# Performance work log

Measured on AMD Instinct MI355X. Metric: run time of the kernel, lower is better.

## Reference

```python
import jax, jax.numpy as jnp
import numpy as np

N_NODES = 50000
N_EDGES = 800000
N_GRAPHS = 2000
D_NODE = 64
D_EDGE = 16
D_MID = 128
N_LAYERS = 3
BN_EPS = 1e-5
LRELU_SLOPE = 0.01


def _bn(h, g, b):
    # training-mode BatchNorm1d: biased batch stats over node dim
    m = jnp.mean(h, axis=0)
    v = jnp.mean((h - m) ** 2, axis=0)
    return (h - m) * jax.lax.rsqrt(v + BN_EPS) * g + b


def _lrelu(h):
    return jnp.where(h >= 0, h, LRELU_SLOPE * h)


def setup_inputs() -> dict:
    key = jax.random.key(0)
    ks = jax.random.split(key, 16)
    s = 0.05
    inp = {
        'x': jax.random.normal(ks[0], (N_NODES, D_NODE), jnp.float32),
        'edge_attr': jax.random.normal(ks[1], (N_EDGES, D_EDGE), jnp.float32),
        'lin_edge_W': jax.random.normal(ks[2], (N_LAYERS, D_EDGE, D_NODE), jnp.float32) * s,
        'lin_edge_b': jax.random.normal(ks[3], (N_LAYERS, D_NODE), jnp.float32) * s,
        'W1': jax.random.normal(ks[4], (N_LAYERS, D_NODE, D_NODE), jnp.float32) * s,
        'b1': jax.random.normal(ks[5], (N_LAYERS, D_NODE), jnp.float32) * s,
        'bn1_g': jnp.ones((N_LAYERS, D_NODE), jnp.float32),
        'bn1_b': jnp.zeros((N_LAYERS, D_NODE), jnp.float32),
        'W2': jax.random.normal(ks[6], (N_LAYERS, D_NODE, D_NODE), jnp.float32) * s,
        'b2': jax.random.normal(ks[7], (N_LAYERS, D_NODE), jnp.float32) * s,
        'eps': jnp.zeros((N_LAYERS,), jnp.float32),
        'obn_g': jnp.ones((N_LAYERS, D_NODE), jnp.float32),
        'obn_b': jnp.zeros((N_LAYERS, D_NODE), jnp.float32),
        'cW1': jax.random.normal(ks[8], (2 * D_NODE, D_MID), jnp.float32) * s,
        'cb1': jax.random.normal(ks[9], (D_MID,), jnp.float32) * s,
        'cbn1_g': jnp.ones((D_MID,), jnp.float32),
        'cbn1_b': jnp.zeros((D_MID,), jnp.float32),
        'cW2': jax.random.normal(ks[10], (D_MID, D_MID), jnp.float32) * s,
        'cb2': jax.random.normal(ks[11], (D_MID,), jnp.float32) * s,
        'cbn2_g': jnp.ones((D_MID,), jnp.float32),
        'cbn2_b': jnp.zeros((D_MID,), jnp.float32),
        'cW3': jax.random.normal(ks[12], (D_MID, 1), jnp.float32) * s,
        'cb3': jax.random.normal(ks[13], (1,), jnp.float32) * s,
        'edge_index': jax.random.randint(ks[14], (2, N_EDGES), 0, N_NODES, jnp.int64 if jax.config.jax_enable_x64 else jnp.int32),
        'batch': jnp.sort(jax.random.randint(ks[15], (N_NODES,), 0, N_GRAPHS, jnp.int64 if jax.config.jax_enable_x64 else jnp.int32)),
    }
    return inp


def reference(x, edge_attr, lin_edge_W, lin_edge_b, W1, b1, bn1_g, bn1_b, W2, b2,
              eps, obn_g, obn_b, cW1, cb1, cbn1_g, cbn1_b, cW2, cb2, cbn2_g,
              cbn2_b, cW3, cb3, edge_index, batch):
    src = edge_index[0]  # source nodes j
    dst = edge_index[1]  # target nodes i
    for l in range(N_LAYERS):
        e = edge_attr @ lin_edge_W[l] + lin_edge_b[l]          # [E, D]
        msg = jax.nn.relu(x[src] + e)                          # [E, D]
        aggr = jax.ops.segment_sum(msg, dst, num_segments=N_NODES)
        h = (1.0 + eps[l]) * x + aggr
        h = _lrelu(_bn(h @ W1[l] + b1[l], bn1_g[l], bn1_b[l])) @ W2[l] + b2[l]
        if l != N_LAYERS - 1:
            h = _bn(h, obn_g[l], obn_b[l])
        x = _lrelu(h)
    pool = jax.ops.segment_sum(x, batch, num_segments=N_GRAPHS)  # [G, D]
    h = jnp.concatenate([x, pool[batch]], axis=1)                # [N, 2D]
    h = _lrelu(_bn(h @ cW1 + cb1, cbn1_g, cbn1_b))               # Dropout = identity (eval)
    h = _lrelu(_bn(h @ cW2 + cb2, cbn2_g, cbn2_b))
    out = h @ cW3 + cb3                                          # [N, 1]
    return out.reshape(-1)
```

## Files before the change

### kernel.cpp

```cpp
#include <hip/hip_runtime.h>

#define NN 50000
#define NE 800000
#define NG 2000
#define BN_EPS 1e-5f
#define NB_SCAN 196
#define NCHUNK 50000

typedef __attribute__((ext_vector_type(8))) short bf16x8;
typedef __attribute__((ext_vector_type(4))) float f32x4;

__device__ __forceinline__ float lrelu(float v) { return v > 0.f ? v : 0.01f * v; }

__device__ __forceinline__ unsigned short f2bf(float x) {
    union { float f; unsigned u; } v; v.f = x;
    unsigned r = v.u + 0x7FFF + ((v.u >> 16) & 1);
    return (unsigned short)(r >> 16);
}
__device__ __forceinline__ float bf2f(unsigned short h) {
    union { unsigned u; float f; } v; v.u = ((unsigned)h) << 16;
    return v.f;
}
__device__ __forceinline__ bf16x8 u4_to_bf(uint4 u) {
    union { uint4 q; bf16x8 b; } c; c.q = u; return c.b;
}

__global__ __launch_bounds__(256) void k_prep(int* __restrict__ p, int n)
{
    int tid = blockIdx.x * 256 + threadIdx.x;
    for (int i = tid; i < n; i += gridDim.x * 256) p[i] = 0;
}

__global__ __launch_bounds__(256) void k_wcvt(
    const float* __restrict__ W1, const float* __restrict__ W2,
    const float* __restrict__ cW1, const float* __restrict__ cW2,
    unsigned short* __restrict__ w1h, unsigned short* __restrict__ w1l,
    unsigned short* __restrict__ w2h, unsigned short* __restrict__ w2l,
    unsigned short* __restrict__ cw1h, unsigned short* __restrict__ cw1l,
    unsigned short* __restrict__ cw2h, unsigned short* __restrict__ cw2l)
{
    int b = blockIdx.x, t = threadIdx.x;
    if (b < 6) {
        const float* s = (b < 3) ? (W1 + b * 4096) : (W2 + (b - 3) * 4096);
        unsigned short* dh = (b < 3) ? (w1h + b * 4096) : (w2h + (b - 3) * 4096);
        unsigned short* dl = (b < 3) ? (w1l + b * 4096) : (w2l + (b - 3) * 4096);
        for (int i = t; i < 4096; i += 256) {
            int k = i >> 6, n = i & 63;
            float v = s[i];
            unsigned short h = f2bf(v);
            dh[n * 64 + k] = h;
            dl[n * 64 + k] = f2bf(v - bf2f(h));
        }
    } else {
        const float* s = (b == 6) ? cW1 : cW2;
        unsigned short* dh = (b == 6) ? cw1h : cw2h;
        unsigned short* dl = (b == 6) ? cw1l : cw2l;
        for (int i = t; i < 16384; i += 256) {
            int k = i >> 7, n = i & 127;
            float v = s[i];
            unsigned short h = f2bf(v);
            dh[n * 128 + k] = h;
            dl[n * 128 + k] = f2bf(v - bf2f(h));
        }
    }
}

__global__ __launch_bounds__(256) void k_hist(const int* __restrict__ dst, int* __restrict__ cnt)
{
    int tid = blockIdx.x * 256 + threadIdx.x;
    for (int e = tid; e < NE; e += gridDim.x * 256) atomicAdd(&cnt[dst[e]], 1);
}

__global__ __launch_bounds__(256) void k_scanA(const int* __restrict__ cnt,
    int* __restrict__ off, int* __restrict__ bsum)
{
    __shared__ int s[256];
    int t = threadIdx.x;
    int i = blockIdx.x * 256 + t;
    int v = (i < NN) ? cnt[i] : 0;
    s[t] = v; __syncthreads();
    #pragma unroll
    for (int d = 1; d < 256; d <<= 1) {
        int u = (t >= d) ? s[t - d] : 0;
        __syncthreads();
        s[t] += u;
        __syncthreads();
    }
    if (i < NN) off[i + 1] = s[t];
    if (t == 255) bsum[blockIdx.x] = s[255];
}

__global__ __launch_bounds__(256) void k_scanB(const int* __restrict__ bsum, int* __restrict__ boff)
{
    __shared__ int s[256];
    int t = threadIdx.x;
    int v = (t < NB_SCAN) ? bsum[t] : 0;
    s[t] = v; __syncthreads();
    #pragma unroll
    for (int d = 1; d < 256; d <<= 1) {
        int u = (t >= d) ? s[t - d] : 0;
        __syncthreads();
        s[t] += u;
        __syncthreads();
    }
    boff[t] = s[t] - v;
}

__global__ __launch_bounds__(256) void k_scanC(const int* __restrict__ cnt,
    int* __restrict__ off, const int* __restrict__ boff, int* __restrict__ cur)
{
    int i = blockIdx.x * 256 + threadIdx.x;
    if (i < NN) {
        int incl = off[i + 1] + boff[blockIdx.x];
        off[i + 1] = incl;
        cur[i] = incl - cnt[i];
    }
    if (i == 0) off[0] = 0;
}

__global__ __launch_bounds__(256) void k_scatter2(
    const int* __restrict__ src, const int* __restrict__ dst,
    int* __restrict__ cur, const float* __restrict__ ea,
    unsigned short* __restrict__ eaz)
{
    int tid = blockIdx.x * 256 + threadIdx.x;
    for (int e = tid; e < NE; e += gridDim.x * 256) {
        int s = src[e], d = dst[e];
        int p = atomicAdd(&cur[d], 1);
        const float4* ap = (const float4*)(ea + (size_t)e * 16);
        float4 a0 = ap[0], a1 = ap[1], a2 = ap[2], a3 = ap[3];
        float v[16] = {a0.x, a0.y, a0.z, a0.w, a1.x, a1.y, a1.z, a1.w,
                       a2.x, a2.y, a2.z, a2.w, a3.x, a3.y, a3.z, a3.w};
        unsigned hi[8], lo[6];
        #pragma unroll
        for (int j = 0; j < 8; ++j) {
            unsigned short h0 = f2bf(v[2 * j]), h1 = f2bf(v[2 * j + 1]);
            hi[j] = (unsigned)h0 | ((unsigned)h1 << 16);
            if (j < 6)
                lo[j] = (unsigned)f2bf(v[2 * j] - bf2f(f2bf(v[2 * j])))
                      | ((unsigned)f2bf(v[2 * j + 1] - bf2f(f2bf(v[2 * j + 1]))) << 16);
        }
        uint4* rec = (uint4*)(eaz + (size_t)p * 32);
        uint4 r0 = {hi[0], hi[1], hi[2], hi[3]};
        uint4 r1 = {hi[4], hi[5], hi[6], hi[7]};
        uint4 r2 = {lo[0], lo[1], lo[2], lo[3]};
        uint4 r3 = {lo[4], lo[5], (unsigned)s, (unsigned)d};
        rec[0] = r0; rec[1] = r1; rec[2] = r2; rec[3] = r3;
    }
}

__global__ __launch_bounds__(256) void k_init(const float* __restrict__ x,
    const float* __restrict__ eps, int layer, float* __restrict__ aggr)
{
    int tid = blockIdx.x * 256 + threadIdx.x;
    float s = 1.f + eps[layer];
    const float4* xv = (const float4*)x;
    float4* av = (float4*)aggr;
    for (int i = tid; i < NN * 16; i += gridDim.x * 256) {
        float4 v = xv[i];
        v.x *= s; v.y *= s; v.z *= s; v.w *= s;
        av[i] = v;
    }
}

__global__ __launch_bounds__(256) void k_aggr_m(
    const float* __restrict__ x, const unsigned short* __restrict__ eaz,
    const float* __restrict__ We, const float* __restrict__ be,
    float* __restrict__ aggr)
{
    __shared__ unsigned short wth[1024], wtl[1024];
    __shared__ float els[4 * 16 * 65];
    int t = threadIdx.x;
    for (int i = t; i < 1024; i += 256) {
        int col = i >> 4, k = i & 15;
        float v = We[k * 64 + col];
        unsigned short h = f2bf(v);
        wth[col * 16 + k] = h;
        wtl[col * 16 + k] = f2bf(v - bf2f(h));
    }
    __syncthreads();

    int lane = t & 63, w = t >> 6;
    float* myels = els + w * (16 * 65);
    int ar = lane & 15;
    int kg = (lane >> 4) & 1;
    bool klive = lane < 32;

    bf16x8 bh[4], bl[4];
    float bias4[4];
    #pragma unroll
    for (int nc = 0; nc < 4; ++nc) {
        int col = nc * 16 + ar;
        uint4 hv = {0, 0, 0, 0}, lv = {0, 0, 0, 0};
        if (klive) {
            hv = *(const uint4*)(wth + col * 16 + kg * 8);
            lv = *(const uint4*)(wtl + col * 16 + kg * 8);
        }
        bh[nc] = u4_to_bf(hv);
        bl[nc] = u4_to_bf(lv);
        bias4[nc] = be[col];
    }

    int cbase0 = (blockIdx.x * 4 + w) * 8;
    for (int ci = 0; ci < 8; ++ci) {
        int chunk = cbase0 + ci;
        if (chunk >= NCHUNK) break;
        int e0 = chunk * 16;
        const unsigned short* rec = eaz + (size_t)(e0 + ar) * 32;

        int2 sdv = *(const int2*)(rec + 28);
        int sl = sdv.x, dl = sdv.y;

        uint4 hv = {0, 0, 0, 0}, lv = {0, 0, 0, 0};
        if (klive) {
            hv = *(const uint4*)(rec + kg * 8);
            lv = *(const uint4*)(rec + 16 + kg * 8);
            if (kg) { lv.z = 0; lv.w = 0; }
        }
        bf16x8 ah = u4_to_bf(hv), al = u4_to_bf(lv);

        float xv[16];
        #pragma unroll
        for (int e = 0; e < 16; ++e) {
            int s_e = __builtin_amdgcn_readlane(sl, e);
            xv[e] = x[(size_t)s_e * 64 + lane];
        }

        #pragma unroll
        for (int nc = 0; nc < 4; ++nc) {
            f32x4 acc;
            acc[0] = bias4[nc]; acc[1] = bias4[nc]; acc[2] = bias4[nc]; acc[3] = bias4[nc];
            acc = __builtin_amdgcn_mfma_f32_16x16x32_bf16(ah, bh[nc], acc, 0, 0, 0);
            acc = __builtin_amdgcn_mfma_f32_16x16x32_bf16(al, bh[nc], acc, 0, 0, 0);
            acc = __builtin_amdgcn_mfma_f32_16x16x32_bf16(ah, bl[nc], acc, 0, 0, 0);
            int rbase = (lane >> 4) * 4;
            #pragma unroll
            for (int r = 0; r < 4; ++r)
                myels[(rbase + r) * 65 + nc * 16 + ar] = acc[r];
        }

        int d = __builtin_amdgcn_readlane(dl, 0);
        float acc = 0.f;
        #pragma unroll
        for (int e = 0; e < 16; ++e) {
            float m = xv[e] + myels[e * 65 + lane];
            m = fmaxf(m, 0.f);
            acc += m;
            int dn = (e < 15) ? __builtin_amdgcn_readlane(dl, e + 1) : -1;
            if (dn != d) {
                atomicAdd(&aggr[(size_t)d * 64 + lane], acc);
                acc = 0.f;
                d = dn;
            }
        }
    }
}

template<int PRE, int POST>
__global__ __launch_bounds__(256) void k_mm64_f(
    const float* __restrict__ in,
    const unsigned short* __restrict__ Wh, const unsigned short* __restrict__ Wl,
    const float* __restrict__ bias, const float* __restrict__ statsIn,
    const float* __restrict__ gIn, const float* __restrict__ bIn,
    float* __restrict__ out, float* __restrict__ statsOut,
    const int* __restrict__ batch, float* __restrict__ pool)
{
    __shared__ unsigned short Ash[64 * 64], Asl[64 * 64];
    __shared__ unsigned short Bsh[64 * 64], Bsl[64 * 64];
    __shared__ float sc[64], sh[64];
    __shared__ float red[4 * 128];
    int t = threadIdx.x;
    int base = blockIdx.x * 64;
    if (PRE && t < 64) {
        float m = statsIn[t] * (1.f / NN);
        float v = statsIn[64 + t] * (1.f / NN) - m * m;
        float s = gIn[t] * rsqrtf(v + BN_EPS);
        sc[t] = s; sh[t] = bIn[t] - m * s;
    }
    for (int i = t; i < 512; i += 256) {
        int n = i >> 3, cb = i & 7;
        ((uint4*)Bsh)[n * 8 + (cb ^ (n & 7))] = ((const uint4*)Wh)[i];
        ((uint4*)Bsl)[n * 8 + (cb ^ (n & 7))] = ((const uint4*)Wl)[i];
    }
    __syncthreads();
    for (int i = t; i < 512; i += 256) {
        int row = i >> 3, cb = i & 7;
        int node = base + row;
        float v[8] = {0.f, 0.f, 0.f, 0.f, 0.f, 0.f, 0.f, 0.f};
        if (node < NN) {
            float4 u0 = *(const float4*)(in + (size_t)node * 64 + cb * 8);
            float4 u1 = *(const float4*)(in + (size_t)node * 64 + cb * 8 + 4);
            v[0] = u0.x; v[1] = u0.y; v[2] = u0.z; v[3] = u0.w;
            v[4] = u1.x; v[5] = u1.y; v[6] = u1.z; v[7] = u1.w;
            if (PRE) {
                #pragma unroll
                for (int j = 0; j < 8; ++j) {
                    int c = cb * 8 + j;
                    v[j] = lrelu(fmaf(v[j], sc[c], sh[c]));
                }
            }
        }
        unsigned hw[4], lw[4];
        #pragma unroll
        for (int j = 0; j < 4; ++j) {
            unsigned short h0 = f2bf(v[2 * j]), h1 = f2bf(v[2 * j + 1]);
            unsigned short l0 = f2bf(v[2 * j] - bf2f(h0)), l1 = f2bf(v[2 * j + 1] - bf2f(h1));
            hw[j] = (unsigned)h0 | ((unsigned)h1 << 16);
            lw[j] = (unsigned)l0 | ((unsigned)l1 << 16);
        }
        uint4 rh = { hw[0], hw[1], hw[2], hw[3] };
        uint4 rl = { lw[0], lw[1], lw[2], lw[3] };
        int idx = row * 8 + (cb ^ (row & 7));
        ((uint4*)Ash)[idx] = rh;
        ((uint4*)Asl)[idx] = rl;
    }
    __syncthreads();

    int w = t >> 6, l = t & 63;
    int ar = l & 15, kg = l >> 4;
    bf16x8 afh[2], afl[2];
    #pragma unroll
    for (int kt = 0; kt < 2; ++kt) {
        int row = w * 16 + ar, cb = kt * 4 + kg;
        int idx = row * 8 + (cb ^ (row & 7));
        afh[kt] = ((const bf16x8*)Ash)[idx];
        afl[kt] = ((const bf16x8*)Asl)[idx];
    }
    f32x4 acc[4];
    #pragma unroll
    for (int nt = 0; nt < 4; ++nt) { acc[nt][0] = 0.f; acc[nt][1] = 0.f; acc[nt][2] = 0.f; acc[nt][3] = 0.f; }
    #pragma unroll
    for (int nt = 0; nt < 4; ++nt) {
        #pragma unroll
        for (int kt = 0; kt < 2; ++kt) {
            int n = nt * 16 + ar, cb = kt * 4 + kg;
            int idx = n * 8 + (cb ^ (n & 7));
            bf16x8 bfh = ((const bf16x8*)Bsh)[idx];
            bf16x8 bfl = ((const bf16x8*)Bsl)[idx];
            acc[nt] = __builtin_amdgcn_mfma_f32_16x16x32_bf16(afh[kt], bfh, acc[nt], 0, 0, 0);
            acc[nt] = __builtin_amdgcn_mfma_f32_16x16x32_bf16(afl[kt], bfh, acc[nt], 0, 0, 0);
            acc[nt] = __builtin_amdgcn_mfma_f32_16x16x32_bf16(afh[kt], bfl, acc[nt], 0, 0, 0);
        }
    }
    int rb = base + w * 16 + kg * 4;
    int bidx[4];
    if (POST == 1) {
        #pragma unroll
        for (int r = 0; r < 4; ++r)
            bidx[r] = (rb + r < NN) ? batch[rb + r] : 0;
    }
    #pragma unroll
    for (int nt = 0; nt < 4; ++nt) {
        int col = nt * 16 + ar;
        float bv = bias[col];
        float s = 0.f, q = 0.f;
        #pragma unroll
        for (int r = 0; r < 4; ++r) {
            int node = rb + r;
            float d = acc[nt][r] + bv;
            if (POST == 1) d = lrelu(d);
            if (node < NN) {
                out[(size_t)node * 64 + col] = d;
                if (POST == 1)
                    atomicAdd(&pool[(size_t)bidx[r] * 64 + col], d);
            }
            if (POST == 0) {
                d = (node < NN) ? d : 0.f;
                s += d; q += d * d;
            }
        }
        if (POST == 0) {
            s += __shfl_xor(s, 16); s += __shfl_xor(s, 32);
            q += __shfl_xor(q, 16); q += __shfl_xor(q, 32);
            if (kg == 0) { red[w * 128 + col] = s; red[w * 128 + 64 + col] = q; }
        }
    }
    if (POST == 0) {
        __syncthreads();
        if (t < 128) {
            int c = t & 63, which = t >> 6;
            float v = red[0 * 128 + which * 64 + c] + red[1 * 128 + which * 64 + c]
                    + red[2 * 128 + which * 64 + c] + red[3 * 128 + which * 64 + c];
            atomicAdd(&statsOut[which * 64 + c], v);
        }
    }
}

template<int MODE>
__global__ __launch_bounds__(256) void k_cmm_f(
    const float* __restrict__ inA, const float* __restrict__ pool,
    const int* __restrict__ batch, const float* __restrict__ statsIn,
    const float* __restrict__ gIn, const float* __restrict__ bIn,
    const unsigned short* __restrict__ Wh, const unsigned short* __restrict__ Wl,
    const float* __restrict__ bias,
    float* __restrict__ out, float* __restrict__ statsOut)
{
    __shared__ unsigned short Ash[64 * 128], Asl[64 * 128];
    __shared__ unsigned short Bsh[64 * 128], Bsl[64 * 128];
    __shared__ float sc[128], sh[128];
    __shared__ float red[4 * 128];
    int t = threadIdx.x;
    int base = (blockIdx.x >> 1) * 64;
    int ncol0 = (blockIdx.x & 1) * 64;
    if (MODE == 1 && t < 128) {
        float m = statsIn[t] * (1.f / NN);
        float v = statsIn[128 + t] * (1.f / NN) - m * m;
        float s = gIn[t] * rsqrtf(v + BN_EPS);
        sc[t] = s; sh[t] = bIn[t] - m * s;
    }
    for (int i = t; i < 1024; i += 256) {
        int n = i >> 4, cb = i & 15;
        int idx = n * 16 + (cb ^ (n & 7));
        ((uint4*)Bsh)[idx] = ((const uint4*)Wh)[(ncol0 + n) * 16 + cb];
        ((uint4*)Bsl)[idx] = ((const uint4*)Wl)[(ncol0 + n) * 16 + cb];
    }
    __syncthreads();
    for (int i = t; i < 1024; i += 256) {
        int row = i >> 4, cb = i & 15;
        int node = base + row;
        float v[8] = {0.f, 0.f, 0.f, 0.f, 0.f, 0.f, 0.f, 0.f};
        if (node < NN) {
            const float* sp;
            if (MODE == 0) {
                sp = (cb < 8) ? (inA + (size_t)node * 64 + cb * 8)
                              : (pool + (size_t)batch[node] * 64 + (cb - 8) * 8);
            } else {
                sp = inA + (size_t)node * 128 + cb * 8;
            }
            float4 u0 = *(const float4*)sp;
            float4 u1 = *(const float4*)(sp + 4);
            v[0] = u0.x; v[1] = u0.y; v[2] = u0.z; v[3] = u0.w;
            v[4] = u1.x; v[5] = u1.y; v[6] = u1.z; v[7] = u1.w;
            if (MODE == 1) {
                #pragma unroll
                for (int j = 0; j < 8; ++j) {
                    int c = cb * 8 + j;
                    v[j] = lrelu(fmaf(v[j], sc[c], sh[c]));
                }
            }
        }
        unsigned hw[4], lw[4];
        #pragma unroll
        for (int j = 0; j < 4; ++j) {
            unsigned short h0 = f2bf(v[2 * j]), h1 = f2bf(v[2 * j + 1]);
            unsigned short l0 = f2bf(v[2 * j] - bf2f(h0)), l1 = f2bf(v[2 * j + 1] - bf2f(h1));
            hw[j] = (unsigned)h0 | ((unsigned)h1 << 16);
            lw[j] = (unsigned)l0 | ((unsigned)l1 << 16);
        }
        uint4 rh = { hw[0], hw[1], hw[2], hw[3] };
        uint4 rl = { lw[0], lw[1], lw[2], lw[3] };
        int idx = row * 16 + (cb ^ (row & 7));
        ((uint4*)Ash)[idx] = rh;
        ((uint4*)Asl)[idx] = rl;
    }
    __syncthreads();

    int w = t >> 6, l = t & 63;
    int ar = l & 15, kg = l >> 4;
    bf16x8 afh[4], afl[4];
    #pragma unroll
    for (int kt = 0; kt < 4; ++kt) {
        int row = w * 16 + ar, cb = kt * 4 + kg;
        int idx = row * 16 + (cb ^ (row & 7));
        afh[kt] = ((const bf16x8*)Ash)[idx];
        afl[kt] = ((const bf16x8*)Asl)[idx];
    }
    f32x4 acc[4];
    #pragma unroll
    for (int nt = 0; nt < 4; ++nt) { acc[nt][0] = 0.f; acc[nt][1] = 0.f; acc[nt][2] = 0.f; acc[nt][3] = 0.f; }
    #pragma unroll
    for (int nt = 0; nt < 4; ++nt) {
        #pragma unroll
        for (int kt = 0; kt < 4; ++kt) {
            int n = nt * 16 + ar, cb = kt * 4 + kg;
            int idx = n * 16 + (cb ^ (n & 7));
            bf16x8 bfh = ((const bf16x8*)Bsh)[idx];
            bf16x8 bfl = ((const bf16x8*)Bsl)[idx];
            acc[nt] = __builtin_amdgcn_mfma_f32_16x16x32_bf16(afh[kt], bfh, acc[nt], 0, 0, 0);
            acc[nt] = __builtin_amdgcn_mfma_f32_16x16x32_bf16(afl[kt], bfh, acc[nt], 0, 0, 0);
            acc[nt] = __builtin_amdgcn_mfma_f32_16x16x32_bf16(afh[kt], bfl, acc[nt], 0, 0, 0);
        }
    }
    int rb = base + w * 16 + kg * 4;
    #pragma unroll
    for (int nt = 0; nt < 4; ++nt) {
        int colg = ncol0 + nt * 16 + ar;
        float bv = bias[colg];
        float s = 0.f, q = 0.f;
        #pragma unroll
        for (int r = 0; r < 4; ++r) {
            int node = rb + r;
            float d = acc[nt][r] + bv;
            if (node < NN) out[(size_t)node * 128 + colg] = d;
            d = (node < NN) ? d : 0.f;
            s += d; q += d * d;
        }
        s += __shfl_xor(s, 16); s += __shfl_xor(s, 32);
        q += __shfl_xor(q, 16); q += __shfl_xor(q, 32);
        int col = nt * 16 + ar;
        if (kg == 0) { red[w * 128 + col] = s; red[w * 128 + 64 + col] = q; }
    }
    __syncthreads();
    if (t < 128) {
        int c = t & 63, which = t >> 6;
        float v = red[0 * 128 + which * 64 + c] + red[1 * 128 + which * 64 + c]
                + red[2 * 128 + which * 64 + c] + red[3 * 128 + which * 64 + c];
        atomicAdd(&statsOut[which * 128 + ncol0 + c], v);
    }
}

__global__ __launch_bounds__(256) void k_bn2(
    const float* __restrict__ in, const float* __restrict__ stats,
    const float* __restrict__ g, const float* __restrict__ b,
    const float* __restrict__ eps, int nextLayer,
    float* __restrict__ xout, float* __restrict__ aggrOut)
{
    int tid = blockIdx.x * 256 + threadIdx.x;
    float e1 = 1.f + eps[nextLayer];
    for (int i = tid; i < NN * 16; i += gridDim.x * 256) {
        int c4 = (i & 15) << 2;
        float4 v = ((const float4*)in)[i];
        float o[4] = {v.x, v.y, v.z, v.w};
        #pragma unroll
        for (int j = 0; j < 4; ++j) {
            int c = c4 + j;
            float m = stats[c] * (1.f / NN);
            float vv = stats[64 + c] * (1.f / NN) - m * m;
            float s = g[c] * rsqrtf(vv + BN_EPS);
            o[j] = lrelu(fmaf(o[j] - m, s, b[c]));
        }
        float4 r = {o[0], o[1], o[2], o[3]};
        ((float4*)xout)[i] = r;
        float4 r2 = {o[0] * e1, o[1] * e1, o[2] * e1, o[3] * e1};
        ((float4*)aggrOut)[i] = r2;
    }
}

__global__ __launch_bounds__(256) void k_out(
    const float* __restrict__ h, const float* __restrict__ stats,
    const float* __restrict__ g, const float* __restrict__ b,
    const float* __restrict__ W3, const float* __restrict__ b3,
    float* __restrict__ outv)
{
    int lane = threadIdx.x & 63;
    int wid = (blockIdx.x * 256 + threadIdx.x) >> 6;
    int nw = (gridDim.x * 256) >> 6;
    float m0 = stats[lane] * (1.f / NN);
    float v0 = stats[128 + lane] * (1.f / NN) - m0 * m0;
    float s0 = g[lane] * rsqrtf(v0 + BN_EPS);
    float h0 = b[lane] - m0 * s0;
    float m1 = stats[64 + lane] * (1.f / NN);
    float v1 = stats[128 + 64 + lane] * (1.f / NN) - m1 * m1;
    float s1 = g[64 + lane] * rsqrtf(v1 + BN_EPS);
    float h1 = b[64 + lane] - m1 * s1;
    float w0 = W3[lane], w1 = W3[64 + lane];
    float bb = b3[0];
    for (int n = wid; n < NN; n += nw) {
        float a = h[(size_t)n * 128 + lane];
        float c = h[(size_t)n * 128 + 64 + lane];
        a = lrelu(fmaf(a, s0, h0));
        c = lrelu(fmaf(c, s1, h1));
        float p = a * w0 + c * w1;
        p += __shfl_xor(p, 32);
        p += __shfl_xor(p, 16);
        p += __shfl_xor(p, 8);
        p += __shfl_xor(p, 4);
        p += __shfl_xor(p, 2);
        p += __shfl_xor(p, 1);
        if (lane == 0) outv[n] = p + bb;
    }
}

extern "C" void kernel_launch(void* const* d_in, const int* in_sizes, int n_in,
                              void* d_out, int out_size, void* d_ws, size_t ws_size,
                              hipStream_t stream)
{
    const float* x0   = (const float*)d_in[0];
    const float* ea   = (const float*)d_in[1];
    const float* leW  = (const float*)d_in[2];
    const float* leb  = (const float*)d_in[3];
    const float* W1   = (const float*)d_in[4];
    const float* b1   = (const float*)d_in[5];
    const float* g1   = (const float*)d_in[6];
    const float* bb1  = (const float*)d_in[7];
    const float* W2   = (const float*)d_in[8];
    const float* b2   = (const float*)d_in[9];
    const float* eps  = (const float*)d_in[10];
    const float* og   = (const float*)d_in[11];
    const float* ob   = (const float*)d_in[12];
    const float* cW1  = (const float*)d_in[13];
    const float* cb1  = (const float*)d_in[14];
    const float* cg1  = (const float*)d_in[15];
    const float* cbb1 = (const float*)d_in[16];
    const float* cW2  = (const float*)d_in[17];
    const float* cb2  = (const float*)d_in[18];
    const float* cg2  = (const float*)d_in[19];
    const float* cbb2 = (const float*)d_in[20];
    const float* cW3  = (const float*)d_in[21];
    const float* cb3  = (const float*)d_in[22];
    const int* ei     = (const int*)d_in[23];
    const int* batch  = (const int*)d_in[24];
    const int* src = ei;
    const int* dst = ei + NE;

    float* xbuf   = (float*)d_ws;
    float* hbuf   = xbuf + (size_t)NN * 64;
    unsigned short* eaz = (unsigned short*)(hbuf + (size_t)NN * 64);
    float* h128   = (float*)eaz;
    float* pool   = (float*)(eaz + (size_t)NE * 32);
    float* cstats = pool + (size_t)NG * 64;
    float* stats  = cstats + 512;
    int*   cnt    = (int*)(stats + 768);
    int*   off    = cnt + NN;
    int*   cur    = off + NN + 4;
    int*   bsum   = cur + NN;
    int*   boff   = bsum + 256;
    unsigned short* w1h  = (unsigned short*)(boff + 256);
    unsigned short* w1l  = w1h + 3 * 4096;
    unsigned short* w2h  = w1l + 3 * 4096;
    unsigned short* w2l  = w2h + 3 * 4096;
    unsigned short* cw1h = w2l + 3 * 4096;
    unsigned short* cw1l = cw1h + 16384;
    unsigned short* cw2h = cw1l + 16384;
    unsigned short* cw2l = cw2h + 16384;
    float* outp   = (float*)d_out;

    int zeroN = NG * 64 + 512 + 768 + NN;

    int fGrid  = (NN + 63) / 64;
    int aGrid  = (NCHUNK + 31) / 32;

    k_prep<<<512, 256, 0, stream>>>((int*)pool, zeroN);
    k_wcvt<<<8, 256, 0, stream>>>(W1, W2, cW1, cW2, w1h, w1l, w2h, w2l,
                                  cw1h, cw1l, cw2h, cw2l);
    k_hist<<<1024, 256, 0, stream>>>(dst, cnt);
    k_scanA<<<NB_SCAN, 256, 0, stream>>>(cnt, off, bsum);
    k_scanB<<<1, 256, 0, stream>>>(bsum, boff);
    k_scanC<<<NB_SCAN, 256, 0, stream>>>(cnt, off, boff, cur);
    k_scatter2<<<2048, 256, 0, stream>>>(src, dst, cur, ea, eaz);

    k_init<<<1024, 256, 0, stream>>>(x0, eps, 0, hbuf);
    for (int l = 0; l < 3; ++l) {
        const float* xc = (l == 0) ? x0 : xbuf;
        float* st = stats + l * 256;
        k_aggr_m<<<aGrid, 256, 0, stream>>>(xc, eaz,
                leW + l * 1024, leb + l * 64, hbuf);
        k_mm64_f<0, 0><<<fGrid, 256, 0, stream>>>(hbuf, w1h + l * 4096, w1l + l * 4096,
                b1 + l * 64, nullptr, nullptr, nullptr, hbuf, st, nullptr, nullptr);
        if (l < 2) {
            k_mm64_f<1, 0><<<fGrid, 256, 0, stream>>>(hbuf, w2h + l * 4096, w2l + l * 4096,
                    b2 + l * 64, st, g1 + l * 64, bb1 + l * 64, hbuf, st + 128,
                    nullptr, nullptr);
            k_bn2<<<1024, 256, 0, stream>>>(hbuf, st + 128, og + l * 64, ob + l * 64,
                    eps, l + 1, xbuf, hbuf);
        } else {
            k_mm64_f<1, 1><<<fGrid, 256, 0, stream>>>(hbuf, w2h + l * 4096, w2l + l * 4096,
                    b2 + l * 64, st, g1 + l * 64, bb1 + l * 64, xbuf, nullptr,
                    batch, pool);
        }
    }
    k_cmm_f<0><<<fGrid * 2, 256, 0, stream>>>(xbuf, pool, batch, nullptr, nullptr, nullptr,
                                              cw1h, cw1l, cb1, h128, cstats);
    k_cmm_f<1><<<fGrid * 2, 256, 0, stream>>>(h128, nullptr, nullptr, cstats, cg1, cbb1,
                                              cw2h, cw2l, cb2, h128, cstats + 256);
    k_out<<<1024, 256, 0, stream>>>(h128, cstats + 256, cg2, cbb2, cW3, cb3, outp);
}
```

Baseline: 544.2 us.

## Compact edge records to 48 bytes and prefetch next chunk in aggregation

Each sorted edge record shrinks from 64 to 48 bytes. Only 6 of the 16 edge features keep a bf16 low-part correction term, and src and dst are packed as two 16-bit indices in one word. The aggregation kernel now software-pipelines its chunks: it loads the next chunk's record and gathers its x rows while the current chunk's MFMA and scatter-add run. This cuts edge-record traffic and hides gather latency, at the cost of more registers and lower precision in the edge linear layer for the features that lost their correction term.

Result: slower. 582.5 us (+7.0%).

```diff
diff --git a/kernel.cpp b/kernel.cpp
--- a/kernel.cpp
+++ b/kernel.cpp
@@ -6,6 +6,7 @@
 #define BN_EPS 1e-5f
 #define NB_SCAN 196
 #define NCHUNK 50000
+#define RECW 24
 
 typedef __attribute__((ext_vector_type(8))) short bf16x8;
 typedef __attribute__((ext_vector_type(4))) float f32x4;
@@ -131,21 +132,21 @@
         float4 a0 = ap[0], a1 = ap[1], a2 = ap[2], a3 = ap[3];
         float v[16] = {a0.x, a0.y, a0.z, a0.w, a1.x, a1.y, a1.z, a1.w,
                        a2.x, a2.y, a2.z, a2.w, a3.x, a3.y, a3.z, a3.w};
-        unsigned hi[8], lo[6];
+        unsigned hi[8], lo[3];
         #pragma unroll
         for (int j = 0; j < 8; ++j) {
             unsigned short h0 = f2bf(v[2 * j]), h1 = f2bf(v[2 * j + 1]);
             hi[j] = (unsigned)h0 | ((unsigned)h1 << 16);
-            if (j < 6)
-                lo[j] = (unsigned)f2bf(v[2 * j] - bf2f(f2bf(v[2 * j])))
-                      | ((unsigned)f2bf(v[2 * j + 1] - bf2f(f2bf(v[2 * j + 1]))) << 16);
-        }
-        uint4* rec = (uint4*)(eaz + (size_t)p * 32);
+            if (j < 3)
+                lo[j] = (unsigned)f2bf(v[2 * j] - bf2f(h0))
+                      | ((unsigned)f2bf(v[2 * j + 1] - bf2f(h1)) << 16);
+        }
+        uint4* rec = (uint4*)(eaz + (size_t)p * RECW);
         uint4 r0 = {hi[0], hi[1], hi[2], hi[3]};
         uint4 r1 = {hi[4], hi[5], hi[6], hi[7]};
-        uint4 r2 = {lo[0], lo[1], lo[2], lo[3]};
-        uint4 r3 = {lo[4], lo[5], (unsigned)s, (unsigned)d};
-        rec[0] = r0; rec[1] = r1; rec[2] = r2; rec[3] = r3;
+        uint4 r2 = {lo[0], lo[1], lo[2],
+                    (unsigned)s | ((unsigned)d << 16)};
+        rec[0] = r0; rec[1] = r1; rec[2] = r2;
     }
 }
 
@@ -202,30 +203,40 @@
     }
 
     int cbase0 = (blockIdx.x * 4 + w) * 8;
-    for (int ci = 0; ci < 8; ++ci) {
-        int chunk = cbase0 + ci;
-        if (chunk >= NCHUNK) break;
-        int e0 = chunk * 16;
-        const unsigned short* rec = eaz + (size_t)(e0 + ar) * 32;
-
-        int2 sdv = *(const int2*)(rec + 28);
-        int sl = sdv.x, dl = sdv.y;
-
-        uint4 hv = {0, 0, 0, 0}, lv = {0, 0, 0, 0};
+    if (cbase0 >= NCHUNK) return;
+    int ncc = NCHUNK - cbase0; if (ncc > 8) ncc = 8;
+
+    auto loadrec = [&](int chunk, uint4& hv, uint4& lv, int& sl, int& dl) {
+        const unsigned short* rec = eaz + (size_t)(chunk * 16 + ar) * RECW;
+        unsigned sdw = *(const unsigned*)(rec + 22);
+        sl = (int)(sdw & 0xFFFFu);
+        dl = (int)(sdw >> 16);
+        uint4 h = {0, 0, 0, 0}, l = {0, 0, 0, 0};
         if (klive) {
-            hv = *(const uint4*)(rec + kg * 8);
-            lv = *(const uint4*)(rec + 16 + kg * 8);
-            if (kg) { lv.z = 0; lv.w = 0; }
-        }
-        bf16x8 ah = u4_to_bf(hv), al = u4_to_bf(lv);
-
-        float xv[16];
-        #pragma unroll
-        for (int e = 0; e < 16; ++e) {
-            int s_e = __builtin_amdgcn_readlane(sl, e);
-            xv[e] = x[(size_t)s_e * 64 + lane];
-        }
-
+            h = *(const uint4*)(rec + kg * 8);
+            if (kg == 0) {
+                uint4 r2 = *(const uint4*)(rec + 16);
+                l.x = r2.x; l.y = r2.y; l.z = r2.z;
+            }
+        }
+        hv = h; lv = l;
+    };
+
+    uint4 hvA, lvA; int slA, dlA;
+    loadrec(cbase0, hvA, lvA, slA, dlA);
+    float xvA[16];
+    #pragma unroll
+    for (int e = 0; e < 16; ++e) {
+        int s_e = __builtin_amdgcn_readlane(slA, e);
+        xvA[e] = x[(size_t)s_e * 64 + lane];
+    }
+
+    for (int ci = 0; ci < ncc; ++ci) {
+        bool more = (ci + 1 < ncc);
+        uint4 hvB = {0,0,0,0}, lvB = {0,0,0,0}; int slB = 0, dlB = 0;
+        if (more) loadrec(cbase0 + ci + 1, hvB, lvB, slB, dlB);
+
+        bf16x8 ah = u4_to_bf(hvA), al = u4_to_bf(lvA);
         #pragma unroll
         for (int nc = 0; nc < 4; ++nc) {
             f32x4 acc;
@@ -239,20 +250,33 @@
                 myels[(rbase + r) * 65 + nc * 16 + ar] = acc[r];
         }
 
-        int d = __builtin_amdgcn_readlane(dl, 0);
+        float xvB[16];
+        if (more) {
+            #pragma unroll
+            for (int e = 0; e < 16; ++e) {
+                int s_e = __builtin_amdgcn_readlane(slB, e);
+                xvB[e] = x[(size_t)s_e * 64 + lane];
+            }
+        }
+
+        int d = __builtin_amdgcn_readlane(dlA, 0);
         float acc = 0.f;
         #pragma unroll
         for (int e = 0; e < 16; ++e) {
-            float m = xv[e] + myels[e * 65 + lane];
+            float m = xvA[e] + myels[e * 65 + lane];
             m = fmaxf(m, 0.f);
             acc += m;
-            int dn = (e < 15) ? __builtin_amdgcn_readlane(dl, e + 1) : -1;
+            int dn = (e < 15) ? __builtin_amdgcn_readlane(dlA, e + 1) : -1;
             if (dn != d) {
                 atomicAdd(&aggr[(size_t)d * 64 + lane], acc);
                 acc = 0.f;
                 d = dn;
             }
         }
+
+        hvA = hvB; lvA = lvB; slA = slB; dlA = dlB;
+        #pragma unroll
+        for (int e = 0; e < 16; ++e) xvA[e] = xvB[e];
     }
 }
 
@@ -607,7 +631,7 @@
     float* hbuf   = xbuf + (size_t)NN * 64;
     unsigned short* eaz = (unsigned short*)(hbuf + (size_t)NN * 64);
     float* h128   = (float*)eaz;
-    float* pool   = (float*)(eaz + (size_t)NE * 32);
+    float* pool   = (float*)(eaz + (size_t)NE * RECW);
     float* cstats = pool + (size_t)NG * 64;
     float* stats  = cstats + 512;
     int*   cnt    = (int*)(stats + 768);
```
